# Optimization experiments

Hardware: AMD Instinct MI355X
Metric: run time of the kernel (lower is better)

Reference implementation:

```python
import jax, jax.numpy as jnp
import numpy as np

B, N, C = 8, 3136, 512
NH, HD = 8, 64
H, W = 56, 56
KS = 5
ALPHA = 4.0
FF = 8 * C


def _safe_pow(x, p):
    # relu(x)**p with well-defined grads at x<=0 (forward identical to torch)
    xs = jnp.where(x > 0, x, 1.0)
    return jnp.where(x > 0, xs ** p, 0.0)


def setup_inputs() -> dict:
    key = jax.random.key(0)
    ks = jax.random.split(key, 12)
    s = 0.02
    return {
        "x": jax.random.normal(ks[0], (B, N, C), jnp.float32),
        "Wqg": jax.random.normal(ks[1], (C, 2 * C), jnp.float32) * s,
        "Wkv": jax.random.normal(ks[2], (C, 2 * C), jnp.float32) * s,
        "pos": jax.random.normal(ks[3], (1, N, C), jnp.float32) * s,
        "scale_p": jax.random.normal(ks[4], (1, 1, C), jnp.float32) * s,
        "power_p": jax.random.normal(ks[5], (1, NH, 1, HD), jnp.float32) * s,
        "dwc_w": jax.random.normal(ks[6], (HD, 1, KS, KS), jnp.float32) * s,
        "dwc_b": jnp.zeros((HD,), jnp.float32),
        "ln_g": jnp.ones((C,), jnp.float32),
        "ln_b": jnp.zeros((C,), jnp.float32),
        "W1": jax.random.normal(ks[7], (C, FF), jnp.float32) * s,
        "b1": jnp.zeros((FF,), jnp.float32),
        "W2": jax.random.normal(ks[8], (FF, C), jnp.float32) * s,
        "b2": jnp.zeros((C,), jnp.float32),
    }


def reference(x, Wqg, Wkv, pos, scale_p, power_p, dwc_w, dwc_b, ln_g, ln_b, W1, b1, W2, b2):
    b, n, c = x.shape
    qg = (x @ Wqg).reshape(b, n, 2, c)
    q, g = qg[:, :, 0], qg[:, :, 1]
    kv = (x @ Wkv).reshape(b, n, 2, c)
    k, v = kv[:, :, 0], kv[:, :, 1]
    k = k + pos

    scale = jax.nn.softplus(scale_p)          # [1,1,C]
    power = 1.0 + ALPHA * jax.nn.sigmoid(power_p)  # [1,NH,1,HD]
    q = q / scale
    k = k / scale

    sh = lambda t: t.reshape(b, n, NH, HD).transpose(0, 2, 1, 3)  # [B,NH,N,HD]
    q, k, v = sh(q), sh(k), sh(v)

    q_pos = _safe_pow(q, power)
    q_neg = _safe_pow(-q, power)
    k_pos = _safe_pow(k, power)
    k_neg = _safe_pow(-k, power)

    q_sim = jnp.concatenate([q_pos, q_neg], -1)  # [B,NH,N,2HD]
    q_opp = jnp.concatenate([q_neg, q_pos], -1)
    kc = jnp.concatenate([k_pos, k_neg], -1)
    v1, v2 = jnp.split(v, 2, axis=-1)            # each [B,NH,N,HD/2]

    km = kc.mean(axis=-2)                        # [B,NH,2HD]
    s = float(n) ** -0.5

    def branch(qf, vf):
        z = 1.0 / (jnp.einsum('bhnd,bhd->bhn', qf, km) + 1e-6)
        kvagg = jnp.einsum('bhnd,bhnm->bhdm', kc * s, vf * s)  # [B,NH,2HD,HD/2]
        return jnp.einsum('bhnd,bhdm->bhnm', qf, kvagg) * z[..., None]

    x_sim = branch(q_sim, v1)
    x_opp = branch(q_opp, v2)
    attn = jnp.concatenate([x_sim, x_opp], -1).transpose(0, 2, 1, 3).reshape(b, n, c)

    # depthwise conv on v viewed as images
    vimg = v.reshape(b * NH, H, W, HD).transpose(0, 3, 1, 2)  # [B*NH,HD,H,W]
    pad = KS // 2
    vconv = jax.lax.conv_general_dilated(vimg, dwc_w, (1, 1), [(pad, pad), (pad, pad)],
                                         feature_group_count=HD)
    vconv = vconv + dwc_b[None, :, None, None]
    vout = vconv.reshape(b, c, n).transpose(0, 2, 1)          # [B,N,C]

    x2 = (attn + vout) * g
    ff = jax.nn.relu(x2 @ W1 + b1) @ W2 + b2
    y = x2 + ff
    mu = y.mean(-1, keepdims=True)
    var = y.var(-1, keepdims=True)
    return (y - mu) / jnp.sqrt(var + 1e-5) * ln_g + ln_b
```

## Files before the change

### kernel.cpp

```cpp
#include <hip/hip_runtime.h>
#include <hip/hip_bf16.h>

#define B_ 8
#define N_ 3136
#define C_ 512
#define NH_ 8
#define HD_ 64
#define FF_ 4096
#define M_ (B_*N_)
#define FFCHUNK 12544

#define SZF 51380224LL
#define SZH 25690112LL
#define OFF_KRAW 0LL
#define OFF_QRAW (OFF_KRAW + SZF)
#define OFF_XB   (OFF_QRAW + SZF)
#define OFF_VB   (OFF_XB + SZH)
#define OFF_ATTN (OFF_VB + SZH)
#define OFF_GX2  (OFF_ATTN + SZH)
#define OFF_WQGT (OFF_GX2 + SZH)
#define OFF_WKVT (OFF_WQGT + 1048576LL)
#define OFF_W1T  (OFF_WKVT + 1048576LL)
#define OFF_W2T  (OFF_W1T + 4194304LL)
#define OFF_KM   (OFF_W2T + 4194304LL)
#define OFF_KVAGG (OFF_KM + 32768LL)
#define OFF_BMAT (OFF_KVAGG + 2097152LL)
#define OFF_Z1   (OFF_BMAT + 2097152LL)
#define OFF_Z2   (OFF_Z1 + 802816LL)
#define OFF_SC   (OFF_Z2 + 802816LL)
#define OFF_PW   (OFF_SC + 2048LL)
#define WS_BYTES (OFF_PW + 2048LL)
#define OFF_H1B  0LL

typedef short bfrag __attribute__((ext_vector_type(8)));
typedef float ffrag __attribute__((ext_vector_type(4)));

__device__ __forceinline__ float safe_pow(float x, float p) {
    return x > 0.f ? powf(x, p) : 0.f;
}

__device__ __forceinline__ void gld_lds16(const void* g, void* l) {
    __builtin_amdgcn_global_load_lds(
        (const __attribute__((address_space(1))) unsigned int*)g,
        (__attribute__((address_space(3))) unsigned int*)l, 16, 0, 0);
}

__global__ void zero_kernel(float* __restrict__ p, long long n) {
    long long i = (long long)blockIdx.x*256 + threadIdx.x;
    if (i < n) p[i] = 0.f;
}

__global__ void prep_params(const float* __restrict__ sp, const float* __restrict__ pp,
                            float* __restrict__ sc, float* __restrict__ pw) {
    int c = blockIdx.x * blockDim.x + threadIdx.x;
    if (c < 512) {
        sc[c] = log1pf(expf(sp[c]));
        pw[c] = 1.f + 4.f / (1.f + expf(-pp[c]));
    }
}

__global__ void cvt_bf16_kernel(const float* __restrict__ s, __hip_bfloat16* __restrict__ d,
                                long long n) {
    long long i = ((long long)blockIdx.x*256 + threadIdx.x)*4;
    if (i < n) {
        float4 v = *(const float4*)(s + i);
        union { __hip_bfloat16 h[4]; uint2 u; } t;
        t.h[0] = __float2bfloat16(v.x);
        t.h[1] = __float2bfloat16(v.y);
        t.h[2] = __float2bfloat16(v.z);
        t.h[3] = __float2bfloat16(v.w);
        *(uint2*)(d + i) = t.u;
    }
}

__global__ __launch_bounds__(256) void transpose_cvt(const float* __restrict__ s,
        __hip_bfloat16* __restrict__ d, int R, int Cc) {
    __shared__ float t[32][33];
    int c0 = blockIdx.x*32, r0 = blockIdx.y*32;
    int tx = threadIdx.x & 31, ty = threadIdx.x >> 5;
#pragma unroll
    for (int i = 0; i < 32; i += 8)
        t[ty+i][tx] = s[(long long)(r0+ty+i)*Cc + c0+tx];
    __syncthreads();
#pragma unroll
    for (int i = 0; i < 32; i += 8)
        d[(long long)(c0+ty+i)*R + r0+tx] = __float2bfloat16(t[tx][ty+i]);
}

template<int EPI>
__global__ __launch_bounds__(256) void gemm_mfma(
    const __hip_bfloat16* __restrict__ A, int lda,
    const __hip_bfloat16* __restrict__ Bt, int ldbt,
    int Ktot, int ldo,
    float* __restrict__ o0, __hip_bfloat16* __restrict__ o1,
    const float* __restrict__ p0, const float* __restrict__ p1)
{
    __shared__ __hip_bfloat16 As[128*32];
    __shared__ __hip_bfloat16 Bs[128*32];
    const int tid = threadIdx.x;
    const int lane = tid & 63, w = tid >> 6;
    const int wm = w >> 1, wn = w & 1;
    const int quad = lane >> 4, l16 = lane & 15;
    const int m0 = blockIdx.y * 128, n0 = blockIdx.x * 128;
    const int srow = lane >> 2;
    const int scol = (lane & 3) * 8;

    ffrag acc[4][4];
#pragma unroll
    for (int i = 0; i < 4; ++i)
#pragma unroll
        for (int j = 0; j < 4; ++j)
#pragma unroll
            for (int r = 0; r < 4; ++r) acc[i][j][r] = 0.f;

    for (int k0 = 0; k0 < Ktot; k0 += 32) {
        __syncthreads();
#pragma unroll
        for (int t = 0; t < 2; ++t) {
            const __hip_bfloat16* gp = A + (long long)(m0 + t*64 + w*16 + srow)*lda + k0 + scol;
            gld_lds16(gp, As + (t*64 + w*16)*32);
        }
#pragma unroll
        for (int t = 0; t < 2; ++t) {
            const __hip_bfloat16* gp = Bt + (long long)(n0 + t*64 + w*16 + srow)*ldbt + k0 + scol;
            gld_lds16(gp, Bs + (t*64 + w*16)*32);
        }
        __syncthreads();
        bfrag af[4], bf[4];
#pragma unroll
        for (int i = 0; i < 4; ++i)
            af[i] = *(const bfrag*)(As + (wm*64 + i*16 + l16)*32 + quad*8);
#pragma unroll
        for (int j = 0; j < 4; ++j)
            bf[j] = *(const bfrag*)(Bs + (wn*64 + j*16 + l16)*32 + quad*8);
#pragma unroll
        for (int i = 0; i < 4; ++i)
#pragma unroll
            for (int j = 0; j < 4; ++j)
                acc[i][j] = __builtin_amdgcn_mfma_f32_16x16x32_bf16(af[i], bf[j], acc[i][j], 0, 0, 0);
    }

#pragma unroll
    for (int i = 0; i < 4; ++i) {
        int rbase = m0 + wm*64 + i*16 + quad*4;
#pragma unroll
        for (int r = 0; r < 4; ++r) {
            long long grow = rbase + r;
            int nmod = 0;
            if constexpr (EPI == 1) nmod = (int)(grow % N_);
#pragma unroll
            for (int j = 0; j < 4; ++j) {
                int gcol = n0 + wn*64 + j*16 + l16;
                float v = acc[i][j][r];
                if constexpr (EPI == 0) {
                    if (gcol < 512) o0[grow*512 + gcol] = v / p0[gcol];
                    else o1[grow*512 + gcol - 512] = __float2bfloat16(v);
                } else if constexpr (EPI == 1) {
                    if (gcol < 512) o0[grow*512 + gcol] = (v + p1[(long long)nmod*512 + gcol]) / p0[gcol];
                    else o1[grow*512 + gcol - 512] = __float2bfloat16(v);
                } else if constexpr (EPI == 2) {
                    o1[grow*(long long)ldo + gcol] = __float2bfloat16(fmaxf(v + p0[gcol], 0.f));
                } else {
                    o0[grow*512 + gcol] = o0[grow*512 + gcol] + v + p0[gcol];
                }
            }
        }
    }
}

__global__ __launch_bounds__(256) void kvagg_kernel(const float* __restrict__ kraw,
                                                    const __hip_bfloat16* __restrict__ vb,
                                                    const float* __restrict__ pw,
                                                    float* __restrict__ km,
                                                    float* __restrict__ kvagg)
{
    int zb = blockIdx.x;
    int b = zb >> 3, h = zb & 7;
    int chunk = blockIdx.y;
    int tid = threadIdx.x;
    __shared__ float kcl[16][128];
    __shared__ float vl[16][64];
    float acc[32];
#pragma unroll
    for (int j = 0; j < 32; ++j) acc[j] = 0.f;
    float kmacc = 0.f;
    const int dd = tid & 63;
    const float p = pw[h*64 + dd];
    const int m = tid & 63, dq = tid >> 6;
    for (int r = 0; r < 13; ++r) {
        int n0 = chunk*196 + r*16;
        int cnt = (r < 12) ? 16 : 4;
        __syncthreads();
#pragma unroll
        for (int i = 0; i < 4; ++i) {
            int nl = (tid >> 6) + i*4;
            if (nl < cnt) {
                long long rb = ((long long)(b*N_ + n0 + nl))*512 + h*64 + dd;
                float kv_ = kraw[rb];
                kcl[nl][dd]      = kv_ > 0.f ? powf(kv_, p) : 0.f;
                kcl[nl][64 + dd] = kv_ < 0.f ? powf(-kv_, p) : 0.f;
                vl[nl][dd] = __bfloat162float(vb[rb]);
            }
        }
        __syncthreads();
        for (int nl = 0; nl < cnt; ++nl) {
            float vm = vl[nl][m];
            const float4* kp = (const float4*)&kcl[nl][dq*32];
#pragma unroll
            for (int j4 = 0; j4 < 8; ++j4) {
                float4 kk = kp[j4];
                acc[j4*4+0] = fmaf(kk.x, vm, acc[j4*4+0]);
                acc[j4*4+1] = fmaf(kk.y, vm, acc[j4*4+1]);
                acc[j4*4+2] = fmaf(kk.z, vm, acc[j4*4+2]);
                acc[j4*4+3] = fmaf(kk.w, vm, acc[j4*4+3]);
            }
        }
        if (tid < 128) {
            for (int nl = 0; nl < cnt; ++nl) kmacc += kcl[nl][tid];
        }
    }
#pragma unroll
    for (int j = 0; j < 32; ++j)
        atomicAdd(&kvagg[(long long)zb*8192 + (dq*32 + j)*64 + m], acc[j]);
    if (tid < 128) atomicAdd(&km[zb*128 + tid], kmacc);
}

__global__ void bmat_kernel(const float* __restrict__ kvagg, float* __restrict__ bmat) {
    int idx = blockIdx.x * 256 + threadIdx.x;
    int z = idx >> 13, r = idx & 8191;
    int d = r >> 6, j = r & 63;
    int sd = (j < 32) ? d : ((d + 64) & 127);
    bmat[idx] = kvagg[((long long)z << 13) + (sd << 6) + j] * (1.0f / (float)N_);
}

__global__ __launch_bounds__(256) void z_kernel(const float* __restrict__ qraw,
                                                const float* __restrict__ pw,
                                                const float* __restrict__ km,
                                                float* __restrict__ z1, float* __restrict__ z2)
{
    int zb = blockIdx.x;
    int b = zb >> 3, h = zb & 7;
    int n0 = blockIdx.y * 64;
    __shared__ float kmn[128];
    __shared__ float q[64][129];
    int tid = threadIdx.x;
    if (tid < 128) kmn[tid] = km[zb*128 + tid] * (1.0f / (float)N_);
    for (int i = tid; i < 64*64; i += 256) {
        int nl = i >> 6, d = i & 63;
        float qv = qraw[((long long)(b*N_ + n0 + nl))*512 + h*64 + d];
        float p = pw[h*64 + d];
        q[nl][d]      = safe_pow(qv, p);
        q[nl][d + 64] = safe_pow(-qv, p);
    }
    __syncthreads();
    int nl = tid >> 2, qtr = tid & 3;
    float p1 = 0.f, p2 = 0.f;
    int d0 = qtr * 32;
    for (int d = d0; d < d0 + 32; ++d) {
        p1 = fmaf(q[nl][d], kmn[d], p1);
        p2 = fmaf(q[nl][(d + 64) & 127], kmn[d], p2);
    }
    p1 += __shfl_xor(p1, 1); p1 += __shfl_xor(p1, 2);
    p2 += __shfl_xor(p2, 1); p2 += __shfl_xor(p2, 2);
    if (qtr == 0) {
        int n = n0 + nl;
        z1[(long long)zb*N_ + n] = 1.0f / (p1 + 1e-6f);
        z2[(long long)zb*N_ + n] = 1.0f / (p2 + 1e-6f);
    }
}

__global__ __launch_bounds__(256) void attn_gemm(const float* __restrict__ qraw,
                                                 const float* __restrict__ bmat,
                                                 const float* __restrict__ pw,
                                                 const float* __restrict__ z1,
                                                 const float* __restrict__ z2,
                                                 __hip_bfloat16* __restrict__ attnb)
{
    int zb = blockIdx.y;
    int b = zb >> 3, h = zb & 7;
    const float* Ab = qraw + (long long)b*N_*512 + h*64;
    const float* Bb = bmat + (long long)zb*8192;
    const float* pwh = pw + h*64;
    const int m0 = blockIdx.x * 64;
    const int tid = threadIdx.x;
    const int ty = tid >> 4, tx = tid & 15;
    const int arow = tid >> 2, acol = (tid & 3) * 4;
    const int brow = tid >> 4, bcol = (tid & 15) * 4;

    __shared__ float As[16][68];
    __shared__ float Bs[16][68];
    float acc[4][4] = {};

    for (int k0 = 0; k0 < 128; k0 += 16) {
        int kk = k0 + acol;
        int kb = kk & 63;
        float4 raw = *(const float4*)(Ab + (long long)(m0 + arow)*512 + kb);
        float sgn = (kk >= 64) ? -1.f : 1.f;
        float4 av;
        av.x = safe_pow(sgn*raw.x, pwh[kb+0]);
        av.y = safe_pow(sgn*raw.y, pwh[kb+1]);
        av.z = safe_pow(sgn*raw.z, pwh[kb+2]);
        av.w = safe_pow(sgn*raw.w, pwh[kb+3]);
        float4 bv = *(const float4*)(Bb + (long long)(k0 + brow)*64 + bcol);
        __syncthreads();
        As[acol+0][arow] = av.x;
        As[acol+1][arow] = av.y;
        As[acol+2][arow] = av.z;
        As[acol+3][arow] = av.w;
        *(float4*)&Bs[brow][bcol] = bv;
        __syncthreads();
#pragma unroll
        for (int kx = 0; kx < 16; ++kx) {
            float4 a4 = *(const float4*)&As[kx][ty*4];
            float4 b4 = *(const float4*)&Bs[kx][tx*4];
            float ar[4] = {a4.x, a4.y, a4.z, a4.w};
            float br[4] = {b4.x, b4.y, b4.z, b4.w};
#pragma unroll
            for (int i = 0; i < 4; ++i)
#pragma unroll
                for (int j = 0; j < 4; ++j)
                    acc[i][j] = fmaf(ar[i], br[j], acc[i][j]);
        }
    }
#pragma unroll
    for (int i = 0; i < 4; ++i) {
        int row = m0 + ty*4 + i;
#pragma unroll
        for (int j = 0; j < 4; ++j) {
            int col = tx*4 + j;
            float zz = ((col < 32) ? z1 : z2)[(long long)zb*N_ + row];
            attnb[((long long)(b*N_ + row))*512 + h*64 + col] = __float2bfloat16(acc[i][j] * zz);
        }
    }
}

__global__ __launch_bounds__(256) void conv_combine(
    const __hip_bfloat16* __restrict__ vb, const float* __restrict__ dwc_w,
    const float* __restrict__ dwc_b, const __hip_bfloat16* __restrict__ attnb,
    __hip_bfloat16* __restrict__ gx2, float* __restrict__ out)
{
    __shared__ __hip_bfloat16 patch[8][32][64];
    __shared__ float wsh[1600];
    __shared__ float bsh[64];
    const int tid = threadIdx.x;
    const int zb = blockIdx.z;
    const int b = zb >> 3, h = zb & 7;
    const int y0 = blockIdx.y * 4;
    const int x0 = blockIdx.x * 28;

    for (int i = tid; i < 1600; i += 256) wsh[i] = dwc_w[i];
    if (tid < 64) bsh[tid] = dwc_b[tid];

    for (int ci = tid; ci < 4096; ci += 256) {
        int c4 = ci & 15;
        int xs = (ci >> 4) & 31;
        int yy = ci >> 9;
        int gy = y0 - 2 + yy, gx = x0 - 2 + xs;
        uint2 val; val.x = 0u; val.y = 0u;
        if ((unsigned)gy < 56u && (unsigned)gx < 56u) {
            long long n = gy*56 + gx;
            val = *(const uint2*)(vb + ((long long)b*N_ + n)*512 + h*64 + c4*4);
        }
        *(uint2*)&patch[yy][xs][c4*4] = val;
    }
    __syncthreads();

    const int c = tid & 63;
    const int xg = tid >> 6;
    float wr[25];
#pragma unroll
    for (int t = 0; t < 25; ++t) wr[t] = wsh[c*25 + t];
    const float bias = bsh[c];
    const int C = h*64 + c;

    for (int yl = 0; yl < 4; ++yl) {
        for (int xi7 = 0; xi7 < 7; ++xi7) {
            int xi = xg*7 + xi7;
            float sum = bias;
#pragma unroll
            for (int ky = 0; ky < 5; ++ky)
#pragma unroll
                for (int kx = 0; kx < 5; ++kx)
                    sum = fmaf(wr[ky*5+kx],
                               __bfloat162float(patch[yl+ky][xi+kx][c]), sum);
            int n = (y0 + yl)*56 + x0 + xi;
            long long row = (long long)b*N_ + n;
            float attn = __bfloat162float(attnb[row*512 + C]);
            float g = __bfloat162float(gx2[row*512 + C]);
            float x2 = (attn + sum) * g;
            out[row*512 + C] = x2;
            gx2[row*512 + C] = __float2bfloat16(x2);
        }
    }
}

__global__ __launch_bounds__(256) void ln_kernel(float* __restrict__ y,
                                                 const float* __restrict__ g,
                                                 const float* __restrict__ bta)
{
    int wid = threadIdx.x >> 6, lane = threadIdx.x & 63;
    long long row = (long long)blockIdx.x*4 + wid;
    float v[8];
    float s = 0.f, s2 = 0.f;
#pragma unroll
    for (int i = 0; i < 8; ++i) {
        v[i] = y[row*512 + i*64 + lane];
        s += v[i];
        s2 = fmaf(v[i], v[i], s2);
    }
#pragma unroll
    for (int o = 32; o > 0; o >>= 1) { s += __shfl_xor(s, o); s2 += __shfl_xor(s2, o); }
    float mu = s * (1.f/512.f);
    float var = s2 * (1.f/512.f) - mu*mu;
    float rstd = rsqrtf(var + 1e-5f);
#pragma unroll
    for (int i = 0; i < 8; ++i) {
        int c = i*64 + lane;
        y[row*512 + c] = (v[i] - mu) * rstd * g[c] + bta[c];
    }
}

extern "C" void kernel_launch(void* const* d_in, const int* in_sizes, int n_in,
                              void* d_out, int out_size, void* d_ws, size_t ws_size,
                              hipStream_t stream)
{
    (void)in_sizes; (void)n_in; (void)out_size;
    if (ws_size < (size_t)WS_BYTES) return;

    const float* x       = (const float*)d_in[0];
    const float* Wqg     = (const float*)d_in[1];
    const float* Wkv     = (const float*)d_in[2];
    const float* pos     = (const float*)d_in[3];
    const float* scale_p = (const float*)d_in[4];
    const float* power_p = (const float*)d_in[5];
    const float* dwc_w   = (const float*)d_in[6];
    const float* dwc_b   = (const float*)d_in[7];
    const float* ln_g    = (const float*)d_in[8];
    const float* ln_b    = (const float*)d_in[9];
    const float* W1      = (const float*)d_in[10];
    const float* b1      = (const float*)d_in[11];
    const float* W2      = (const float*)d_in[12];
    const float* b2      = (const float*)d_in[13];
    float* out = (float*)d_out;
    char* ws   = (char*)d_ws;

    float* kraw  = (float*)(ws + OFF_KRAW);
    float* qraw  = (float*)(ws + OFF_QRAW);
    __hip_bfloat16* xb   = (__hip_bfloat16*)(ws + OFF_XB);
    __hip_bfloat16* vb   = (__hip_bfloat16*)(ws + OFF_VB);
    __hip_bfloat16* attnb= (__hip_bfloat16*)(ws + OFF_ATTN);
    __hip_bfloat16* gx2  = (__hip_bfloat16*)(ws + OFF_GX2);
    __hip_bfloat16* Wqgt = (__hip_bfloat16*)(ws + OFF_WQGT);
    __hip_bfloat16* Wkvt = (__hip_bfloat16*)(ws + OFF_WKVT);
    __hip_bfloat16* W1t  = (__hip_bfloat16*)(ws + OFF_W1T);
    __hip_bfloat16* W2t  = (__hip_bfloat16*)(ws + OFF_W2T);
    __hip_bfloat16* h1b  = (__hip_bfloat16*)(ws + OFF_H1B);
    float* km    = (float*)(ws + OFF_KM);
    float* kvagg = (float*)(ws + OFF_KVAGG);
    float* bmat  = (float*)(ws + OFF_BMAT);
    float* z1    = (float*)(ws + OFF_Z1);
    float* z2    = (float*)(ws + OFF_Z2);
    float* sc    = (float*)(ws + OFF_SC);
    float* pw    = (float*)(ws + OFF_PW);

    prep_params<<<2, 256, 0, stream>>>(scale_p, power_p, sc, pw);
    zero_kernel<<<(64*128 + 64*8192 + 255)/256, 256, 0, stream>>>(km, 64*128 + 64*8192);
    cvt_bf16_kernel<<<(int)(((long long)M_*512/4 + 255)/256), 256, 0, stream>>>(x, xb, (long long)M_*512);
    transpose_cvt<<<dim3(32, 16), 256, 0, stream>>>(Wqg, Wqgt, 512, 1024);
    transpose_cvt<<<dim3(32, 16), 256, 0, stream>>>(Wkv, Wkvt, 512, 1024);
    transpose_cvt<<<dim3(128, 16), 256, 0, stream>>>(W1, W1t, 512, 4096);
    transpose_cvt<<<dim3(16, 128), 256, 0, stream>>>(W2, W2t, 4096, 512);

    gemm_mfma<0><<<dim3(8, 196), 256, 0, stream>>>(xb, 512, Wqgt, 512, 512, 0,
                                                   qraw, gx2, sc, nullptr);
    gemm_mfma<1><<<dim3(8, 196), 256, 0, stream>>>(xb, 512, Wkvt, 512, 512, 0,
                                                   kraw, vb, sc, pos);

    kvagg_kernel<<<dim3(64, 16), 256, 0, stream>>>(kraw, vb, pw, km, kvagg);
    bmat_kernel<<<2048, 256, 0, stream>>>(kvagg, bmat);
    z_kernel<<<dim3(64, 49), 256, 0, stream>>>(qraw, pw, km, z1, z2);
    attn_gemm<<<dim3(49, 64), 256, 0, stream>>>(qraw, bmat, pw, z1, z2, attnb);

    conv_combine<<<dim3(2, 14, 64), 256, 0, stream>>>(vb, dwc_w, dwc_b, attnb, gx2, out);

    for (int c = 0; c < 2; ++c) {
        const __hip_bfloat16* x2c = gx2 + (long long)c*FFCHUNK*512;
        float* outc = out + (long long)c*FFCHUNK*512;
        gemm_mfma<2><<<dim3(32, FFCHUNK/128), 256, 0, stream>>>(
            x2c, 512, W1t, 512, 512, 4096, nullptr, h1b, b1, nullptr);
        gemm_mfma<3><<<dim3(4, FFCHUNK/128), 256, 0, stream>>>(
            h1b, 4096, W2t, 4096, 4096, 0, outc, nullptr, b2, nullptr);
    }

    ln_kernel<<<6272, 256, 0, stream>>>(out, ln_g, ln_b);
}
```

Baseline: 1.218 ms.

## Compute K-V aggregation with bf16 MFMA via precomputed transposed kc buffer

```diff
diff --git a/kernel.cpp b/kernel.cpp
--- a/kernel.cpp
+++ b/kernel.cpp
@@ -12,9 +12,9 @@
 
 #define SZF 51380224LL
 #define SZH 25690112LL
-#define OFF_KRAW 0LL
-#define OFF_QRAW (OFF_KRAW + SZF)
-#define OFF_XB   (OFF_QRAW + SZF)
+#define OFF_A    0LL
+#define OFF_KCT  (OFF_A + SZF)
+#define OFF_XB   (OFF_KCT + SZF)
 #define OFF_VB   (OFF_XB + SZH)
 #define OFF_ATTN (OFF_VB + SZH)
 #define OFF_GX2  (OFF_ATTN + SZH)
@@ -23,8 +23,7 @@
 #define OFF_W1T  (OFF_WKVT + 1048576LL)
 #define OFF_W2T  (OFF_W1T + 4194304LL)
 #define OFF_KM   (OFF_W2T + 4194304LL)
-#define OFF_KVAGG (OFF_KM + 32768LL)
-#define OFF_BMAT (OFF_KVAGG + 2097152LL)
+#define OFF_BMAT (OFF_KM + 32768LL)
 #define OFF_Z1   (OFF_BMAT + 2097152LL)
 #define OFF_Z2   (OFF_Z1 + 802816LL)
 #define OFF_SC   (OFF_Z2 + 802816LL)
@@ -168,69 +167,125 @@
     }
 }
 
-__global__ __launch_bounds__(256) void kvagg_kernel(const float* __restrict__ kraw,
-                                                    const __hip_bfloat16* __restrict__ vb,
-                                                    const float* __restrict__ pw,
-                                                    float* __restrict__ km,
-                                                    float* __restrict__ kvagg)
-{
-    int zb = blockIdx.x;
+__global__ __launch_bounds__(256) void kc_kernel(const float* __restrict__ kraw,
+        const float* __restrict__ pw, __hip_bfloat16* __restrict__ kcT,
+        float* __restrict__ km)
+{
+    __shared__ float kt[64][68];
+    int zb = blockIdx.x, nt = blockIdx.y;
     int b = zb >> 3, h = zb & 7;
-    int chunk = blockIdx.y;
+    int n0 = nt * 64;
     int tid = threadIdx.x;
-    __shared__ float kcl[16][128];
-    __shared__ float vl[16][64];
-    float acc[32];
-#pragma unroll
-    for (int j = 0; j < 32; ++j) acc[j] = 0.f;
-    float kmacc = 0.f;
-    const int dd = tid & 63;
-    const float p = pw[h*64 + dd];
-    const int m = tid & 63, dq = tid >> 6;
-    for (int r = 0; r < 13; ++r) {
-        int n0 = chunk*196 + r*16;
-        int cnt = (r < 12) ? 16 : 4;
+    {
+        int r = tid >> 2, q = (tid & 3) * 16;
+        const float* src = kraw + ((long long)(b*N_ + n0 + r))*512 + h*64 + q;
+        float4 a0 = *(const float4*)(src);
+        float4 a1 = *(const float4*)(src + 4);
+        float4 a2 = *(const float4*)(src + 8);
+        float4 a3 = *(const float4*)(src + 12);
+        *(float4*)&kt[r][q]      = a0;
+        *(float4*)&kt[r][q + 4]  = a1;
+        *(float4*)&kt[r][q + 8]  = a2;
+        *(float4*)&kt[r][q + 12] = a3;
+    }
+    __syncthreads();
+    int d2 = tid >> 1, half = tid & 1;
+    int d = d2 & 63;
+    bool neg = d2 >= 64;
+    float p = pw[h*64 + d];
+    float kms = 0.f;
+    union { __hip_bfloat16 h8[32]; uint4 u[4]; } buf;
+#pragma unroll
+    for (int i = 0; i < 32; ++i) {
+        float kv = kt[half*32 + i][d];
+        float x = neg ? -kv : kv;
+        float kc = x > 0.f ? powf(x, p) : 0.f;
+        kms += kc;
+        buf.h8[i] = __float2bfloat16(kc);
+    }
+    __hip_bfloat16* dst = kcT + ((long long)zb*128 + d2)*N_ + n0 + half*32;
+    *(uint4*)(dst)      = buf.u[0];
+    *(uint4*)(dst + 8)  = buf.u[1];
+    *(uint4*)(dst + 16) = buf.u[2];
+    *(uint4*)(dst + 24) = buf.u[3];
+    kms += __shfl_xor(kms, 1);
+    if (half == 0) atomicAdd(&km[zb*128 + d2], kms);
+}
+
+__global__ __launch_bounds__(256) void kvagg_mfma(
+    const __hip_bfloat16* __restrict__ kcT,
+    const __hip_bfloat16* __restrict__ vb,
+    float* __restrict__ part)
+{
+    __shared__ __hip_bfloat16 vlds[32*66];
+    const int ks = blockIdx.x;
+    const int zb = blockIdx.y;
+    const int b = zb >> 3, h = zb & 7;
+    const int tid = threadIdx.x;
+    const int lane = tid & 63, w = tid >> 6;
+    const int quad = lane >> 4, l16 = lane & 15;
+    const int vrow = tid >> 3, vchunk = tid & 7;
+
+    ffrag acc[2][4];
+#pragma unroll
+    for (int i = 0; i < 2; ++i)
+#pragma unroll
+        for (int j = 0; j < 4; ++j)
+#pragma unroll
+            for (int r = 0; r < 4; ++r) acc[i][j][r] = 0.f;
+
+    const __hip_bfloat16* Abase = kcT + (long long)zb*128*N_;
+
+    for (int s = 0; s < 14; ++s) {
+        int klo = ks*448 + s*32;
+        uint4 vv = *(const uint4*)(vb + ((long long)(b*N_ + klo + vrow))*512 + h*64 + vchunk*8);
         __syncthreads();
-#pragma unroll
-        for (int i = 0; i < 4; ++i) {
-            int nl = (tid >> 6) + i*4;
-            if (nl < cnt) {
-                long long rb = ((long long)(b*N_ + n0 + nl))*512 + h*64 + dd;
-                float kv_ = kraw[rb];
-                kcl[nl][dd]      = kv_ > 0.f ? powf(kv_, p) : 0.f;
-                kcl[nl][64 + dd] = kv_ < 0.f ? powf(-kv_, p) : 0.f;
-                vl[nl][dd] = __bfloat162float(vb[rb]);
-            }
+        {
+            unsigned* dp = (unsigned*)&vlds[vrow*66 + vchunk*8];
+            dp[0] = vv.x; dp[1] = vv.y; dp[2] = vv.z; dp[3] = vv.w;
         }
         __syncthreads();
-        for (int nl = 0; nl < cnt; ++nl) {
-            float vm = vl[nl][m];
-            const float4* kp = (const float4*)&kcl[nl][dq*32];
-#pragma unroll
-            for (int j4 = 0; j4 < 8; ++j4) {
-                float4 kk = kp[j4];
-                acc[j4*4+0] = fmaf(kk.x, vm, acc[j4*4+0]);
-                acc[j4*4+1] = fmaf(kk.y, vm, acc[j4*4+1]);
-                acc[j4*4+2] = fmaf(kk.z, vm, acc[j4*4+2]);
-                acc[j4*4+3] = fmaf(kk.w, vm, acc[j4*4+3]);
-            }
-        }
-        if (tid < 128) {
-            for (int nl = 0; nl < cnt; ++nl) kmacc += kcl[nl][tid];
-        }
-    }
-#pragma unroll
-    for (int j = 0; j < 32; ++j)
-        atomicAdd(&kvagg[(long long)zb*8192 + (dq*32 + j)*64 + m], acc[j]);
-    if (tid < 128) atomicAdd(&km[zb*128 + tid], kmacc);
-}
-
-__global__ void bmat_kernel(const float* __restrict__ kvagg, float* __restrict__ bmat) {
+        bfrag af[2], bf[4];
+#pragma unroll
+        for (int i = 0; i < 2; ++i)
+            af[i] = *(const bfrag*)(Abase + ((long long)(w*32 + i*16 + l16))*N_ + klo + quad*8);
+#pragma unroll
+        for (int j = 0; j < 4; ++j) {
+            bfrag t;
+#pragma unroll
+            for (int jj = 0; jj < 8; ++jj)
+                t[jj] = *(const short*)&vlds[(quad*8 + jj)*66 + j*16 + l16];
+            bf[j] = t;
+        }
+#pragma unroll
+        for (int i = 0; i < 2; ++i)
+#pragma unroll
+            for (int j = 0; j < 4; ++j)
+                acc[i][j] = __builtin_amdgcn_mfma_f32_16x16x32_bf16(af[i], bf[j], acc[i][j], 0, 0, 0);
+    }
+
+    long long pbase = ((long long)ks*64 + zb)*8192;
+#pragma unroll
+    for (int i = 0; i < 2; ++i)
+#pragma unroll
+        for (int r = 0; r < 4; ++r) {
+            int d2 = w*32 + i*16 + quad*4 + r;
+#pragma unroll
+            for (int j = 0; j < 4; ++j)
+                part[pbase + d2*64 + j*16 + l16] = acc[i][j][r];
+        }
+}
+
+__global__ void bmat_kernel(const float* __restrict__ part, float* __restrict__ bmat) {
     int idx = blockIdx.x * 256 + threadIdx.x;
     int z = idx >> 13, r = idx & 8191;
     int d = r >> 6, j = r & 63;
     int sd = (j < 32) ? d : ((d + 64) & 127);
-    bmat[idx] = kvagg[((long long)z << 13) + (sd << 6) + j] * (1.0f / (float)N_);
+    float s = 0.f;
+#pragma unroll
+    for (int ks = 0; ks < 7; ++ks)
+        s += part[((long long)ks*64 + z)*8192 + (sd << 6) + j];
+    bmat[idx] = s * (1.0f / (float)N_);
 }
 
 __global__ __launch_bounds__(256) void z_kernel(const float* __restrict__ qraw,
@@ -444,11 +499,12 @@
     float* out = (float*)d_out;
     char* ws   = (char*)d_ws;
 
-    float* kraw  = (float*)(ws + OFF_KRAW);
-    float* qraw  = (float*)(ws + OFF_QRAW);
+    float* abuf  = (float*)(ws + OFF_A);
+    __hip_bfloat16* kcT  = (__hip_bfloat16*)(ws + OFF_KCT);
     __hip_bfloat16* xb   = (__hip_bfloat16*)(ws + OFF_XB);
     __hip_bfloat16* vb   = (__hip_bfloat16*)(ws + OFF_VB);
     __hip_bfloat16* attnb= (__hip_bfloat16*)(ws + OFF_ATTN);
+    float* part  = (float*)(ws + OFF_ATTN);
     __hip_bfloat16* gx2  = (__hip_bfloat16*)(ws + OFF_GX2);
     __hip_bfloat16* Wqgt = (__hip_bfloat16*)(ws + OFF_WQGT);
     __hip_bfloat16* Wkvt = (__hip_bfloat16*)(ws + OFF_WKVT);
@@ -456,7 +512,6 @@
     __hip_bfloat16* W2t  = (__hip_bfloat16*)(ws + OFF_W2T);
     __hip_bfloat16* h1b  = (__hip_bfloat16*)(ws + OFF_H1B);
     float* km    = (float*)(ws + OFF_KM);
-    float* kvagg = (float*)(ws + OFF_KVAGG);
     float* bmat  = (float*)(ws + OFF_BMAT);
     float* z1    = (float*)(ws + OFF_Z1);
     float* z2    = (float*)(ws + OFF_Z2);
@@ -464,22 +519,24 @@
     float* pw    = (float*)(ws + OFF_PW);
 
     prep_params<<<2, 256, 0, stream>>>(scale_p, power_p, sc, pw);
-    zero_kernel<<<(64*128 + 64*8192 + 255)/256, 256, 0, stream>>>(km, 64*128 + 64*8192);
+    zero_kernel<<<32, 256, 0, stream>>>(km, 64*128);
     cvt_bf16_kernel<<<(int)(((long long)M_*512/4 + 255)/256), 256, 0, stream>>>(x, xb, (long long)M_*512);
     transpose_cvt<<<dim3(32, 16), 256, 0, stream>>>(Wqg, Wqgt, 512, 1024);
     transpose_cvt<<<dim3(32, 16), 256, 0, stream>>>(Wkv, Wkvt, 512, 1024);
     transpose_cvt<<<dim3(128, 16), 256, 0, stream>>>(W1, W1t, 512, 4096);
     transpose_cvt<<<dim3(16, 128), 256, 0, stream>>>(W2, W2t, 4096, 512);
 
+    gemm_mfma<1><<<dim3(8, 196), 256, 0, stream>>>(xb, 512, Wkvt, 512, 512, 0,
+                                                   abuf, vb, sc, pos);
+    kc_kernel<<<dim3(64, 49), 256, 0, stream>>>(abuf, pw, kcT, km);
+    kvagg_mfma<<<dim3(7, 64), 256, 0, stream>>>(kcT, vb, part);
+    bmat_kernel<<<2048, 256, 0, stream>>>(part, bmat);
+
     gemm_mfma<0><<<dim3(8, 196), 256, 0, stream>>>(xb, 512, Wqgt, 512, 512, 0,
-                                                   qraw, gx2, sc, nullptr);
-    gemm_mfma<1><<<dim3(8, 196), 256, 0, stream>>>(xb, 512, Wkvt, 512, 512, 0,
-                                                   kraw, vb, sc, pos);
-
-    kvagg_kernel<<<dim3(64, 16), 256, 0, stream>>>(kraw, vb, pw, km, kvagg);
-    bmat_kernel<<<2048, 256, 0, stream>>>(kvagg, bmat);
-    z_kernel<<<dim3(64, 49), 256, 0, stream>>>(qraw, pw, km, z1, z2);
-    attn_gemm<<<dim3(49, 64), 256, 0, stream>>>(qraw, bmat, pw, z1, z2, attnb);
+                                                   abuf, gx2, sc, nullptr);
+
+    z_kernel<<<dim3(64, 49), 256, 0, stream>>>(abuf, pw, km, z1, z2);
+    attn_gemm<<<dim3(49, 64), 256, 0, stream>>>(abuf, bmat, pw, z1, z2, attnb);
 
     conv_combine<<<dim3(2, 14, 64), 256, 0, stream>>>(vb, dwc_w, dwc_b, attnb, gx2, out);
 
```

Result: slower. 1.263 ms (+3.7%).
